# Performance work log

Measured on AMD Instinct MI355X. Metric: run time of the kernel, lower is better.

Reference implementation:

```python
import jax, jax.numpy as jnp
import numpy as np

TAU = 0.5
THRESHOLD = 1.0
V_RESET = 0.0


def setup_inputs() -> dict:
    key = jax.random.key(0)
    T, B, D = 512, 64, 1024
    x = jax.random.normal(key, (T, B, D), dtype=jnp.float32)
    v0 = jnp.zeros((D,), dtype=jnp.float32)  # initial membrane potential, broadcasts over batch
    return {"x": x, "v0": v0}


def reference(x, v0):
    # x: [T, B, D] input current per timestep; v0: [D] initial potential.
    # Faithful LIF update per timestep: v = tau*v + x; spike = (v >= thr);
    # v = v*(1-spike) + v_reset*spike.  Sequential state carried by lax.scan.
    B, D = x.shape[1], x.shape[2]
    v_init = jnp.broadcast_to(v0, (B, D))

    def step(v, xt):
        v = TAU * v + xt
        spike = (v >= THRESHOLD).astype(xt.dtype)
        v = v * (1.0 - spike) + V_RESET * spike
        return v, spike

    _, spikes = jax.lax.scan(step, v_init, x)
    return spikes  # [T, B, D]
```

## Files before the change

kernel.cpp:

```cpp
#include <hip/hip_runtime.h>


constexpr int T_STEPS = 512;
constexpr int B_DIM   = 64;
constexpr int D_DIM   = 1024;
constexpr int N_CHAIN = B_DIM * D_DIM;

__global__ __launch_bounds__(256)
void lif_scan_kernel(const float* __restrict__ x,
                     const float* __restrict__ v0,
                     float* __restrict__ out) {
    const int tid = blockIdx.x * blockDim.x + threadIdx.x;
    const int d   = tid & (D_DIM - 1);

    float v = v0[d];

    const float* xp = x   + tid;
    float*       op = out + tid;

#pragma unroll 16
    for (int t = 0; t < T_STEPS; ++t) {
        const float xt = xp[(size_t)t * N_CHAIN];
        v = v * 0.5f + xt;
        const bool s = (v >= 1.0f);
        op[(size_t)t * N_CHAIN] = s ? 1.0f : 0.0f;
        v = s ? 0.0f : v;
    }
}

extern "C" void kernel_launch(void* const* d_in, const int* in_sizes, int n_in,
                              void* d_out, int out_size, void* d_ws, size_t ws_size,
                              hipStream_t stream) {
    const float* x   = (const float*)d_in[0];
    const float* v0  = (const float*)d_in[1];
    float*       out = (float*)d_out;

    dim3 block(256);
    dim3 grid(N_CHAIN / 256);
    hipLaunchKernelGGL(lif_scan_kernel, grid, block, 0, stream, x, v0, out);
}
```

Baseline: 231.8 us.

## Triple-buffer timestep loads in registers with scheduled prefetch and nontemporal stores

Replaces the simple unrolled time loop with a three-buffer register pipeline. Each thread prefetches blocks of 16 timesteps of input two blocks ahead, and scheduling barriers keep the compiler from reordering the loads and compute. Output spikes are written with nontemporal stores so they bypass the cache. This is meant to keep more loads in flight per thread and hide memory latency, at the cost of more VGPRs and possibly lower occupancy.

```diff
diff --git a/kernel.cpp b/kernel.cpp
--- a/kernel.cpp
+++ b/kernel.cpp
@@ -5,6 +5,8 @@
 constexpr int B_DIM   = 64;
 constexpr int D_DIM   = 1024;
 constexpr int N_CHAIN = B_DIM * D_DIM;
+constexpr int U       = 16;
+constexpr int NB      = T_STEPS / U;
 
 __global__ __launch_bounds__(256)
 void lif_scan_kernel(const float* __restrict__ x,
@@ -18,14 +20,43 @@
     const float* xp = x   + tid;
     float*       op = out + tid;
 
-#pragma unroll 16
-    for (int t = 0; t < T_STEPS; ++t) {
-        const float xt = xp[(size_t)t * N_CHAIN];
-        v = v * 0.5f + xt;
-        const bool s = (v >= 1.0f);
-        op[(size_t)t * N_CHAIN] = s ? 1.0f : 0.0f;
-        v = s ? 0.0f : v;
+    float b0[U], b1[U], b2[U];
+
+#define LOADB(BUF, BLK)                                                     \
+    _Pragma("unroll")                                                       \
+    for (int u = 0; u < U; ++u)                                             \
+        BUF[u] = xp[(size_t)((BLK) * U + u) * N_CHAIN];                     \
+    __builtin_amdgcn_sched_barrier(0);
+
+#define CONSB(BUF, BLK)                                                     \
+    _Pragma("unroll")                                                       \
+    for (int u = 0; u < U; ++u) {                                           \
+        v = v * 0.5f + BUF[u];                        \
+        const bool s = (v >= 1.0f);                                         \
+        __builtin_nontemporal_store(s ? 1.0f : 0.0f,                        \
+                                    op + (size_t)((BLK) * U + u) * N_CHAIN);\
+        v = s ? 0.0f : v;                                                   \
+    }                                                                       \
+    __builtin_amdgcn_sched_barrier(0);
+
+    LOADB(b0, 0)
+    LOADB(b1, 1)
+
+    for (int j = 0; j < 10; ++j) {
+        const int c = 3 * j;
+        LOADB(b2, c + 2)
+        CONSB(b0, c)
+        LOADB(b0, c + 3)
+        CONSB(b1, c + 1)
+        LOADB(b1, c + 4)
+        CONSB(b2, c + 2)
     }
+
+    CONSB(b0, 30)
+    CONSB(b1, 31)
+
+#undef LOADB
+#undef CONSB
 }
 
 extern "C" void kernel_launch(void* const* d_in, const int* in_sizes, int n_in,
```

New measurement: 226.5 us. 2.3% less time.

## Split time scan into warm-started chunks with float4 vector loads and nontemporal stores

Applied to the files above, without the earlier changes.

Splits the 512-step time scan into 4 independent chunks across blocks. Each later chunk rebuilds its state by running 64 warm-up steps from zero, which relies on the 0.5 decay making the starting state vanish below float precision. Each thread now handles 4 adjacent chains using float4 loads, and spikes are written with nontemporal stores. The aim is to shorten the serial dependency chain and raise memory-level parallelism, at the cost of re-reading some input for warm-up and a tiny approximation risk in the carried state.

```diff
diff --git a/kernel.cpp b/kernel.cpp
--- a/kernel.cpp
+++ b/kernel.cpp
@@ -1,30 +1,66 @@
 #include <hip/hip_runtime.h>
 
 
-constexpr int T_STEPS = 512;
-constexpr int B_DIM   = 64;
-constexpr int D_DIM   = 1024;
-constexpr int N_CHAIN = B_DIM * D_DIM;
+constexpr int T_STEPS  = 512;
+constexpr int B_DIM    = 64;
+constexpr int D_DIM    = 1024;
+constexpr int N_CHAIN  = B_DIM * D_DIM;
+constexpr int VEC      = 4;
+constexpr int NT_VEC   = N_CHAIN / VEC;
+constexpr int C_CHUNKS = 4;
+constexpr int T_CHUNK  = T_STEPS / C_CHUNKS;
+constexpr int K_WARM   = 64;
+
+typedef float v4f __attribute__((ext_vector_type(4)));
 
 __global__ __launch_bounds__(256)
 void lif_scan_kernel(const float* __restrict__ x,
                      const float* __restrict__ v0,
                      float* __restrict__ out) {
-    const int tid = blockIdx.x * blockDim.x + threadIdx.x;
-    const int d   = tid & (D_DIM - 1);
+    const int col   = ((blockIdx.x & 63) << 8) + threadIdx.x;
+    const int chunk = blockIdx.x >> 6;
 
-    float v = v0[d];
+    const v4f* xp = (const v4f*)x   + col;
+    v4f*       op = (v4f*)      out + col;
 
-    const float* xp = x   + tid;
-    float*       op = out + tid;
+    const int d0 = (col * VEC) & (D_DIM - 1);
+
+    float v[VEC];
+    const int tstart = chunk * T_CHUNK;
+
+    if (chunk == 0) {
+        const v4f vi = *(const v4f*)(v0 + d0);
+        v[0] = vi.x; v[1] = vi.y; v[2] = vi.z; v[3] = vi.w;
+    } else {
+#pragma unroll
+        for (int i = 0; i < VEC; ++i) v[i] = 0.0f;
+#pragma unroll 16
+        for (int t = tstart - K_WARM; t < tstart; ++t) {
+            const v4f xv = xp[(size_t)t * NT_VEC];
+            const float xs[VEC] = {xv.x, xv.y, xv.z, xv.w};
+#pragma unroll
+            for (int i = 0; i < VEC; ++i) {
+                float vi = v[i] * 0.5f + xs[i];
+                v[i] = (vi >= 1.0f) ? 0.0f : vi;
+            }
+        }
+    }
 
 #pragma unroll 16
-    for (int t = 0; t < T_STEPS; ++t) {
-        const float xt = xp[(size_t)t * N_CHAIN];
-        v = v * 0.5f + xt;
-        const bool s = (v >= 1.0f);
-        op[(size_t)t * N_CHAIN] = s ? 1.0f : 0.0f;
-        v = s ? 0.0f : v;
+    for (int t = tstart; t < tstart + T_CHUNK; ++t) {
+        const v4f xv = xp[(size_t)t * NT_VEC];
+        const float xs[VEC] = {xv.x, xv.y, xv.z, xv.w};
+        float ss[VEC];
+#pragma unroll
+        for (int i = 0; i < VEC; ++i) {
+            float vi = v[i] * 0.5f + xs[i];
+            const bool sp = (vi >= 1.0f);
+            ss[i] = sp ? 1.0f : 0.0f;
+            v[i]  = sp ? 0.0f : vi;
+        }
+        v4f s;
+        s.x = ss[0]; s.y = ss[1]; s.z = ss[2]; s.w = ss[3];
+        __builtin_nontemporal_store(s, op + (size_t)t * NT_VEC);
     }
 }
 
@@ -36,6 +72,6 @@
     float*       out = (float*)d_out;
 
     dim3 block(256);
-    dim3 grid(N_CHAIN / 256);
+    dim3 grid(C_CHUNKS * (NT_VEC / 256));
     hipLaunchKernelGGL(lif_scan_kernel, grid, block, 0, stream, x, v0, out);
 }
```

New measurement: 238.5 us. 2.9% more time.
